# Kernel optimization log

Hardware: AMD Instinct MI355X
Metric: run time of the kernel (lower is better)

## Reference

```python
import jax, jax.numpy as jnp
import numpy as np

N, E, G = 50000, 800000, 64          # nodes, edges, graphs in batch
F, HG, HL = 64, 128, 128             # node feat, graph hidden, lin hidden
AVG_LOG = float(np.log(9.0))         # from deg histogram [0]*8+[1]: log(8+1)


def setup_inputs() -> dict:
    key = jax.random.key(0)
    ks = jax.random.split(key, 24)
    def w(k, shape):
        return 0.1 * jax.random.normal(k, shape, jnp.float32)
    return {
        "x": jax.random.normal(ks[0], (N, F), jnp.float32),
        "edge_index": jax.random.randint(ks[1], (2, E), 0, N),
        "edge_attr": jax.random.normal(ks[2], (E, 1), jnp.float32),
        "batch": jnp.sort(jax.random.randint(ks[3], (N,), 0, G)),
        # PNAConv params (towers=1, pre_layers=1, post_layers=1, edge_dim=1)
        "W_edge": w(ks[4], (1, F)),      "b_edge": w(ks[5], (F,)),
        "W_pre": w(ks[6], (3 * F, F)),   "b_pre": w(ks[7], (F,)),
        "W_post": w(ks[8], (13 * F, HG)), "b_post": w(ks[9], (HG,)),
        "W_lin": w(ks[10], (HG, HG)),    "b_lin": w(ks[11], (HG,)),
        # bn1 / fc2 / bn2
        "g1": jnp.ones((HG,)), "be1": jnp.zeros((HG,)),
        "W2": w(ks[12], (HG, HL)), "b2": w(ks[13], (HL,)),
        "g2": jnp.ones((HL,)), "be2": jnp.zeros((HL,)),
        # one resnet block: fc/bn/fc/bn
        "Wr1": w(ks[14], (HL, HL)), "br1": w(ks[15], (HL,)),
        "gr1": jnp.ones((HL,)), "ber1": jnp.zeros((HL,)),
        "Wr2": w(ks[16], (HL, HL)), "br2": w(ks[17], (HL,)),
        "gr2": jnp.ones((HL,)), "ber2": jnp.zeros((HL,)),
        "W_out": w(ks[18], (HL, 1)), "b_out": w(ks[19], (1,)),
    }


def _bn(z, g, b):
    # BatchNorm1d, training mode: biased batch stats, eps=1e-5
    mu = z.mean(0)
    var = ((z - mu) ** 2).mean(0)
    return (z - mu) * jax.lax.rsqrt(var + 1e-5) * g + b


def _pna(x, edge_index, edge_attr, W_edge, b_edge, W_pre, b_pre,
         W_post, b_post, W_lin, b_lin):
    src, dst = edge_index[0], edge_index[1]  # messages flow j->i, aggregate at dst
    e = edge_attr @ W_edge + b_edge                               # [E, F]
    m = jnp.concatenate([x[dst], x[src], e], -1) @ W_pre + b_pre  # [E, F]
    ones_e = jnp.ones((m.shape[0],), m.dtype)
    cnt = jax.ops.segment_sum(ones_e, dst, N)                     # in-degree
    cnt1 = jnp.maximum(cnt, 1.0)
    mean = jax.ops.segment_sum(m, dst, N) / cnt1[:, None]
    mean2 = jax.ops.segment_sum(m * m, dst, N) / cnt1[:, None]
    std = jnp.sqrt(jax.nn.relu(mean2 - mean * mean) + 1e-5)
    has = (cnt > 0)[:, None]
    mn = jnp.where(has, jax.ops.segment_min(m, dst, N), 0.0)
    mx = jnp.where(has, jax.ops.segment_max(m, dst, N), 0.0)
    agg = jnp.concatenate([mean, mn, mx, std], -1)                # [N, 4F]
    amp = (jnp.log(cnt1 + 1.0) / AVG_LOG)[:, None]                # amplification scaler
    out = jnp.concatenate([agg, agg * amp, agg / amp], -1)        # [N, 12F]
    out = jnp.concatenate([x, out], -1) @ W_post + b_post         # [N, HG]
    return out @ W_lin + b_lin                                    # [N, HG]


def reference(x, edge_index, edge_attr, batch,
              W_edge, b_edge, W_pre, b_pre, W_post, b_post, W_lin, b_lin,
              g1, be1, W2, b2, g2, be2,
              Wr1, br1, gr1, ber1, Wr2, br2, gr2, ber2,
              W_out, b_out):
    h = _pna(x, edge_index, edge_attr, W_edge, b_edge, W_pre, b_pre,
             W_post, b_post, W_lin, b_lin)
    # global_mean_pool over graphs
    gc = jnp.maximum(jax.ops.segment_sum(jnp.ones((h.shape[0],), h.dtype), batch, G), 1.0)
    z = jax.ops.segment_sum(h, batch, G) / gc[:, None]            # [G, HG]
    z = jax.nn.relu(_bn(z, g1, be1))
    z = jax.nn.relu(_bn(z @ W2 + b2, g2, be2))
    r = z
    z = jax.nn.relu(_bn(z @ Wr1 + br1, gr1, ber1))
    z = jax.nn.relu(_bn(z @ Wr2 + br2, gr2, ber2) + r)
    return z @ W_out + b_out                                      # [G, 1]
```

## Files before the change

kernel.cpp:

```cpp
#include <hip/hip_runtime.h>
#include <hip/hip_bf16.h>

using bf16 = __hip_bfloat16;

#define F 64
#define HG 128
#define HL 128
#define AVG_LOG_INV 0.45511961331341866f
#define BSH 5
#define BNODES 32
#define BCAP 1024
#define BTILE 8192
#define NBMAX 1664
#define NBTMAX 128

typedef short short8 __attribute__((ext_vector_type(8)));
typedef float floatx4 __attribute__((ext_vector_type(4)));

__device__ __forceinline__ float b2f(bf16 v) { return __bfloat162float(v); }
__device__ __forceinline__ bf16 f2b(float v) { return __float2bfloat16(v); }
__device__ __forceinline__ short f2bs(float v) { bf16 h = f2b(v); return *(short*)&h; }

__device__ __forceinline__ unsigned packbf2(float x, float y) {
    bf16 a = f2b(x), b = f2b(y);
    unsigned short ua = *(unsigned short*)&a, ub = *(unsigned short*)&b;
    return ((unsigned)ub << 16) | (unsigned)ua;
}

__device__ __forceinline__ float wave_sum(float v) {
    #pragma unroll
    for (int m = 32; m > 0; m >>= 1) v += __shfl_xor(v, m);
    return v;
}

__global__ __launch_bounds__(512) void k_prep(
    const float* __restrict__ x, const float* __restrict__ W_pre,
    bf16* __restrict__ AB, int N,
    const int* __restrict__ ei, const float* __restrict__ ea,
    int* __restrict__ ofs, int2* __restrict__ gout, int E,
    float* __restrict__ gfeat, int* __restrict__ gcnt,
    int NB, int GF, int G, int NBT,
    const float* __restrict__ W_edge, const float* __restrict__ b_edge,
    const float* __restrict__ b_pre, float* __restrict__ uc) {
    __shared__ __align__(16) char smem[18432];
    int t = threadIdx.x;
    int gtid = blockIdx.x * 512 + t;
    int gstr = gridDim.x * 512;
    for (int i = gtid; i < GF; i += gstr) gfeat[i] = 0.f;
    for (int i = gtid; i < G; i += gstr) gcnt[i] = 0;

    if (blockIdx.x < NBT) {
        int* hist = (int*)smem;
        int* aux  = hist + NBMAX;
        int p = blockIdx.x;
        for (int i = t; i < NB; i += 512) hist[i] = 0;
        __syncthreads();
        int base = p * BTILE;
        int lim = E - base; if (lim > BTILE) lim = BTILE;
        int nq = lim >> 2;
        const int4* dst4 = (const int4*)(ei + E + base);
        for (int q = t; q < nq; q += 512) {
            int4 d = dst4[q];
            atomicAdd(&hist[d.x >> BSH], 1);
            atomicAdd(&hist[d.y >> BSH], 1);
            atomicAdd(&hist[d.z >> BSH], 1);
            atomicAdd(&hist[d.w >> BSH], 1);
        }
        for (int i = (nq << 2) + t; i < lim; i += 512)
            atomicAdd(&hist[ei[E + base + i] >> BSH], 1);
        __syncthreads();
        int b0 = t * 4;
        int c0 = 0, c1 = 0, c2 = 0, c3 = 0;
        if (b0 < NB)     c0 = hist[b0];
        if (b0 + 1 < NB) c1 = hist[b0 + 1];
        if (b0 + 2 < NB) c2 = hist[b0 + 2];
        if (b0 + 3 < NB) c3 = hist[b0 + 3];
        int tot = c0 + c1 + c2 + c3;
        aux[t] = tot;
        __syncthreads();
        for (int d = 1; d < 512; d <<= 1) {
            int v = (t >= d) ? aux[t - d] : 0;
            __syncthreads();
            aux[t] += v;
            __syncthreads();
        }
        int run = aux[t] - tot;
        __syncthreads();
        size_t orow = (size_t)p * (NB + 1);
        if (b0 < NB)     { hist[b0]     = run; ofs[orow + b0]     = run; run += c0; }
        if (b0 + 1 < NB) { hist[b0 + 1] = run; ofs[orow + b0 + 1] = run; run += c1; }
        if (b0 + 2 < NB) { hist[b0 + 2] = run; ofs[orow + b0 + 2] = run; run += c2; }
        if (b0 + 3 < NB) { hist[b0 + 3] = run; ofs[orow + b0 + 3] = run; run += c3; }
        if (t == 0) ofs[orow + NB] = lim;
        for (int i = t; i < NB; i += 512) aux[i] = 0;
        __syncthreads();
        const int4* src4 = (const int4*)(ei + base);
        const float4* ea4 = (const float4*)(ea + base);
        int2* seg = gout + (size_t)p * BTILE;
        for (int q = t; q < nq; q += 512) {
            int4 s = src4[q], d = dst4[q];
            float4 v = ea4[q];
            int bb, pos;
            bb = d.x >> BSH; pos = hist[bb] + atomicAdd(&aux[bb], 1);
            seg[pos] = make_int2((d.x << 16) | s.x, __float_as_int(v.x));
            bb = d.y >> BSH; pos = hist[bb] + atomicAdd(&aux[bb], 1);
            seg[pos] = make_int2((d.y << 16) | s.y, __float_as_int(v.y));
            bb = d.z >> BSH; pos = hist[bb] + atomicAdd(&aux[bb], 1);
            seg[pos] = make_int2((d.z << 16) | s.z, __float_as_int(v.z));
            bb = d.w >> BSH; pos = hist[bb] + atomicAdd(&aux[bb], 1);
            seg[pos] = make_int2((d.w << 16) | s.w, __float_as_int(v.w));
        }
        for (int i = (nq << 2) + t; i < lim; i += 512) {
            int s = ei[base + i], d = ei[E + base + i];
            int bb = d >> BSH;
            int pos = hist[bb] + atomicAdd(&aux[bb], 1);
            seg[pos] = make_int2((d << 16) | s, __float_as_int(ea[base + i]));
        }
    } else {
        if (blockIdx.x == NBT && t < 64) {
            int f = t;
            float u = 0.f, c = b_pre[f];
            for (int k = 0; k < 64; k++) {
                float w3 = W_pre[(128 + k) * 64 + f];
                u += W_edge[k] * w3;
                c += b_edge[k] * w3;
            }
            uc[f] = u; uc[64 + f] = c;
        }
        unsigned short* wt = (unsigned short*)smem;
        for (int idx = t; idx < 8192; idx += 512) {
            int k = idx >> 7, m = idx & 127;
            float v = W_pre[((m & 64) + k) * 64 + (m & 63)];
            wt[m * 72 + k] = (unsigned short)f2bs(v);
        }
        __syncthreads();

        int lane = t & 63;
        int row = lane & 15, quad = lane >> 4;
        int w = (blockIdx.x - NBT) * 8 + (t >> 6);
        int nwaves = (gridDim.x - NBT) * 8;
        int ntiles = (N + 15) >> 4;

        for (int tile = w; tile < ntiles; tile += nwaves) {
            int m0 = tile << 4;
            int node_a = m0 + row; if (node_a >= N) node_a = N - 1;
            short8 a[2];
            #pragma unroll
            for (int h = 0; h < 2; h++) {
                const float* xp = x + (size_t)node_a * 64 + h * 32 + quad * 8;
                floatx4 v0 = *(const floatx4*)xp;
                floatx4 v1 = *(const floatx4*)(xp + 4);
                #pragma unroll
                for (int j = 0; j < 4; j++) { a[h][j] = f2bs(v0[j]); a[h][4 + j] = f2bs(v1[j]); }
            }
            #pragma unroll
            for (int tt = 0; tt < 8; tt++) {
                int fbase = tt * 16;
                floatx4 c = {0.f, 0.f, 0.f, 0.f};
                #pragma unroll
                for (int h = 0; h < 2; h++) {
                    short8 bfr = *(const short8*)(wt + (fbase + row) * 72 + h * 32 + quad * 8);
                    c = __builtin_amdgcn_mfma_f32_16x16x32_bf16(a[h], bfr, c, 0, 0, 0);
                }
                #pragma unroll
                for (int r = 0; r < 4; r++) {
                    int node = m0 + quad * 4 + r;
                    if (node < N) AB[(size_t)node * 128 + fbase + row] = f2b(c[r]);
                }
            }
        }
    }
}

__global__ __launch_bounds__(512) void k_edge(
    const bf16* __restrict__ AB, const int2* __restrict__ gout,
    const int* __restrict__ ofs, const float* __restrict__ uc,
    const int* __restrict__ batch, const float* __restrict__ x,
    float* __restrict__ gfeat, int* __restrict__ gcnt,
    int N, int NB, int NBT) {
    __shared__ int2 recs[BCAP], sortd[BCAP];
    __shared__ int ncnt[BNODES], nofs[BNODES], nrank[BNODES];
    __shared__ int gid[BNODES];
    __shared__ unsigned lstat[BNODES][128];
    __shared__ float lamp[BNODES], liamp[BNODES];
    __shared__ int runlo[NBTMAX], runlen[NBTMAX], runpre[NBTMAX];
    __shared__ int etot_s;
    int t = threadIdx.x;
    int b = blockIdx.x;
    int nn = N - b * BNODES; if (nn > BNODES) nn = BNODES;

    if (t < NBTMAX) { runlo[t] = 0; runlen[t] = 0; }
    if (t < BNODES) {
        ncnt[t] = 0; nrank[t] = 0;
        if (t < nn) gid[t] = batch[b * BNODES + t];
    }
    __syncthreads();
    if (t < NBT) {
        int lo = ofs[(size_t)t * (NB + 1) + b];
        int hi = ofs[(size_t)t * (NB + 1) + b + 1];
        runlo[t] = lo; runlen[t] = hi - lo;
    }
    __syncthreads();
    if (t < NBTMAX) runpre[t] = runlen[t];
    __syncthreads();
    for (int d = 1; d < NBTMAX; d <<= 1) {
        int v = 0;
        if (t < NBTMAX && t >= d) v = runpre[t - d];
        __syncthreads();
        if (t < NBTMAX) runpre[t] += v;
        __syncthreads();
    }
    if (t == NBTMAX - 1) etot_s = runpre[NBTMAX - 1];
    int ex = 0;
    if (t < NBTMAX) ex = runpre[t] - runlen[t];
    __syncthreads();
    if (t < NBTMAX) runpre[t] = ex;
    __syncthreads();
    int ecnt = etot_s; if (ecnt > BCAP) ecnt = BCAP;
    for (int i = t; i < ecnt; i += 512) {
        int lo2 = 0, hi2 = NBT;
        while (hi2 - lo2 > 1) {
            int mid = (lo2 + hi2) >> 1;
            if (runpre[mid] <= i) lo2 = mid; else hi2 = mid;
        }
        recs[i] = gout[(size_t)lo2 * BTILE + runlo[lo2] + (i - runpre[lo2])];
    }
    __syncthreads();
    for (int i = t; i < ecnt; i += 512)
        atomicAdd(&ncnt[((unsigned)recs[i].x >> 16) & (BNODES - 1)], 1);
    __syncthreads();
    if (t < BNODES) {
        int v = ncnt[t], inc = v;
        #pragma unroll
        for (int m = 1; m < BNODES; m <<= 1) { int u = __shfl_up(inc, m); if (t >= m) inc += u; }
        nofs[t] = inc - v;
    }
    __syncthreads();
    for (int i = t; i < ecnt; i += 512) {
        int2 r = recs[i];
        int nl = ((unsigned)r.x >> 16) & (BNODES - 1);
        int k = atomicAdd(&nrank[nl], 1);
        sortd[nofs[nl] + k] = r;
    }
    __syncthreads();

    int lane = t & 63, w = t >> 6;
    int half = lane & 31, hi32 = lane >> 5;
    float2 u2 = *(const float2*)(uc + 2 * half);
    float2 c2 = *(const float2*)(uc + 64 + 2 * half);

    for (int nl = w; nl < nn; nl += 8) {
        int n = b * BNODES + nl;
        int lo = nofs[nl], cnt = ncnt[nl], hi = lo + cnt;

        unsigned apack = *(const unsigned*)(AB + (size_t)n * 128 + 2 * half);
        float acx = __uint_as_float(apack << 16) + c2.x;
        float acy = __uint_as_float(apack & 0xffff0000u) + c2.y;

        float sx = 0.f, sy = 0.f, qx = 0.f, qy = 0.f;
        float mnx = 3.4e38f, mny = 3.4e38f, mxx = -3.4e38f, mxy = -3.4e38f;

        auto acc2 = [&](unsigned bp, float eav) {
            float bx = __uint_as_float(bp << 16);
            float by = __uint_as_float(bp & 0xffff0000u);
            float m0 = fmaf(eav, u2.x, acx) + bx;
            float m1 = fmaf(eav, u2.y, acy) + by;
            sx += m0; qx = fmaf(m0, m0, qx);
            sy += m1; qy = fmaf(m1, m1, qy);
            mnx = fminf(mnx, m0); mxx = fmaxf(mxx, m0);
            mny = fminf(mny, m1); mxy = fmaxf(mxy, m1);
        };
        auto gaddr = [&](int sn) {
            return (const unsigned*)(AB + (size_t)sn * 128 + 64 + 2 * half);
        };

        for (int base = lo; base < hi; base += 64) {
            int nb = hi - base; if (nb > 64) nb = 64;
            int2 rec = (lane < nb) ? sortd[base + lane] : make_int2(0, 0);
            int vsn = rec.x & 0xFFFF;
            float vea = __int_as_float(rec.y);
            int i = 0;
            for (; i + 8 <= nb; i += 8) {
                int sn0 = __shfl(vsn, i + hi32);
                int sn1 = __shfl(vsn, i + 2 + hi32);
                int sn2 = __shfl(vsn, i + 4 + hi32);
                int sn3 = __shfl(vsn, i + 6 + hi32);
                float e0 = __shfl(vea, i + hi32);
                float e1 = __shfl(vea, i + 2 + hi32);
                float e2 = __shfl(vea, i + 4 + hi32);
                float e3 = __shfl(vea, i + 6 + hi32);
                unsigned b0 = *gaddr(sn0);
                unsigned b1 = *gaddr(sn1);
                unsigned b2 = *gaddr(sn2);
                unsigned b3 = *gaddr(sn3);
                acc2(b0, e0); acc2(b1, e1); acc2(b2, e2); acc2(b3, e3);
            }
            for (; i + 2 <= nb; i += 2) {
                int   sn = __shfl(vsn, i + hi32);
                float ev = __shfl(vea, i + hi32);
                acc2(*gaddr(sn), ev);
            }
            if (i < nb) {
                int   sn = __shfl(vsn, i);
                float ev = __shfl(vea, i);
                unsigned bp = *gaddr(sn);
                if (hi32 == 0) acc2(bp, ev);
            }
        }
        sx += __shfl_xor(sx, 32); sy += __shfl_xor(sy, 32);
        qx += __shfl_xor(qx, 32); qy += __shfl_xor(qy, 32);
        mnx = fminf(mnx, __shfl_xor(mnx, 32)); mny = fminf(mny, __shfl_xor(mny, 32));
        mxx = fmaxf(mxx, __shfl_xor(mxx, 32)); mxy = fmaxf(mxy, __shfl_xor(mxy, 32));

        float c1 = (cnt > 0) ? (float)cnt : 1.f;
        float inv = 1.f / c1;
        float mex = sx * inv, mey = sy * inv;
        float vx = qx * inv - mex * mex; if (vx < 0.f) vx = 0.f;
        float vy = qy * inv - mey * mey; if (vy < 0.f) vy = 0.f;
        float sdx = sqrtf(vx + 1e-5f), sdy = sqrtf(vy + 1e-5f);
        if (cnt == 0) { mnx = mny = mxx = mxy = 0.f; }

        if (hi32 == 0) {
            lstat[nl][half]      = packbf2(mex, mey);
            lstat[nl][32 + half] = packbf2(mnx, mny);
        } else {
            lstat[nl][64 + half] = packbf2(mxx, mxy);
            lstat[nl][96 + half] = packbf2(sdx, sdy);
        }
        if (lane == 0) {
            float amp = logf(c1 + 1.f) * AVG_LOG_INV;
            lamp[nl] = amp; liamp[nl] = 1.f / amp;
        }
    }
    __syncthreads();

    if (t < 128) {
        int c = t;
        int elem = ((c >> 5) << 6) + ((c & 31) << 1);
        float s1x = 0.f, s1y = 0.f, s2x = 0.f, s2y = 0.f, s3x = 0.f, s3y = 0.f;
        float sxv = 0.f;
        int cnt = 0;
        int cur = gid[0];
        for (int nl = 0; nl < nn; nl++) {
            int g = gid[nl];
            if (g != cur) {
                float* gf = gfeat + (size_t)cur * 832;
                unsafeAtomicAdd(&gf[64 + elem], s1x);
                unsafeAtomicAdd(&gf[65 + elem], s1y);
                unsafeAtomicAdd(&gf[320 + elem], s2x);
                unsafeAtomicAdd(&gf[321 + elem], s2y);
                unsafeAtomicAdd(&gf[576 + elem], s3x);
                unsafeAtomicAdd(&gf[577 + elem], s3y);
                if (t < 64) unsafeAtomicAdd(&gf[t], sxv);
                if (t == 0) atomicAdd(&gcnt[cur], cnt);
                s1x = s1y = s2x = s2y = s3x = s3y = 0.f; sxv = 0.f; cnt = 0;
                cur = g;
            }
            unsigned p = lstat[nl][c];
            float bx = __uint_as_float(p << 16);
            float by = __uint_as_float(p & 0xffff0000u);
            float a = lamp[nl], ia = liamp[nl];
            s1x += bx; s2x = fmaf(bx, a, s2x); s3x = fmaf(bx, ia, s3x);
            s1y += by; s2y = fmaf(by, a, s2y); s3y = fmaf(by, ia, s3y);
            if (t < 64) sxv += x[(size_t)(b * BNODES + nl) * 64 + t];
            cnt++;
        }
        float* gf = gfeat + (size_t)cur * 832;
        unsafeAtomicAdd(&gf[64 + elem], s1x);
        unsafeAtomicAdd(&gf[65 + elem], s1y);
        unsafeAtomicAdd(&gf[320 + elem], s2x);
        unsafeAtomicAdd(&gf[321 + elem], s2y);
        unsafeAtomicAdd(&gf[576 + elem], s3x);
        unsafeAtomicAdd(&gf[577 + elem], s3y);
        if (t < 64) unsafeAtomicAdd(&gf[t], sxv);
        if (t == 0) atomicAdd(&gcnt[cur], cnt);
    }
}

__global__ void k_post1(const float* __restrict__ gfeat, const int* __restrict__ gcnt,
                        const float* __restrict__ W_post, const float* __restrict__ b_post,
                        const float* __restrict__ W_lin, const float* __restrict__ b_lin,
                        float* __restrict__ Zin) {
    int g = blockIdx.x, t = threadIdx.x;
    int j = t & 127, h = t >> 7;
    __shared__ float feat[832];
    __shared__ float part[256];
    __shared__ float z1[128];
    int cg = gcnt[g];
    float r = 1.f / ((cg > 0) ? (float)cg : 1.f);
    for (int i = t; i < 832; i += 256) feat[i] = gfeat[(size_t)g * 832 + i] * r;
    __syncthreads();
    float acc = (h == 0) ? b_post[j] : 0.f;
    const float* Wp = W_post + (size_t)(h * 416) * 128 + j;
    const float* fp = feat + h * 416;
    #pragma unroll 8
    for (int k = 0; k < 416; k++) acc += fp[k] * Wp[(size_t)k * 128];
    part[t] = acc;
    __syncthreads();
    if (t < 128) z1[j] = part[j] + part[128 + j];
    __syncthreads();
    float a2 = (h == 0) ? b_lin[j] : 0.f;
    #pragma unroll
    for (int k = 0; k < 64; k++) a2 += z1[h * 64 + k] * W_lin[(h * 64 + k) * 128 + j];
    part[t] = a2;
    __syncthreads();
    if (t < 128) {
        float v = part[j] + part[128 + j];
        if (cg == 0) v = 0.f;
        Zin[g * 128 + j] = v;
    }
}

__global__ void k_mlpcol(const float* __restrict__ in, const float* __restrict__ W,
                         const float* __restrict__ bias,
                         const float* __restrict__ gamma, const float* __restrict__ beta,
                         const float* __restrict__ res,
                         const float* __restrict__ g_in, const float* __restrict__ be_in,
                         float* __restrict__ outp) {
    __shared__ float A[64 * 129];
    __shared__ float part[4 * 64];
    int t = threadIdx.x;
    int j = blockIdx.x;

    for (int i = t; i < 8192; i += 256) A[(i >> 7) * 129 + (i & 127)] = in[i];
    __syncthreads();

    if (g_in) {
        if (t < 128) {
            int c = t;
            float mu = 0.f;
            for (int r = 0; r < 64; r++) mu += A[r * 129 + c];
            mu *= (1.f / 64.f);
            float var = 0.f;
            for (int r = 0; r < 64; r++) { float d = A[r * 129 + c] - mu; var += d * d; }
            var *= (1.f / 64.f);
            float sc = rsqrtf(var + 1e-5f) * g_in[c], sh = be_in[c];
            for (int r = 0; r < 64; r++) {
                float v = (A[r * 129 + c] - mu) * sc + sh;
                A[r * 129 + c] = v > 0.f ? v : 0.f;
            }
        }
        __syncthreads();
    }

    int r = t & 63, q = t >> 6;
    float acc = 0.f;
    int k0 = q * 32;
    #pragma unroll
    for (int k = 0; k < 32; k++) acc += A[r * 129 + k0 + k] * W[(k0 + k) * 128 + j];
    part[q * 64 + r] = acc;
    __syncthreads();

    if (t < 64) {
        float v = part[t] + part[64 + t] + part[128 + t] + part[192 + t] + bias[j];
        float mu = wave_sum(v) * (1.f / 64.f);
        float d = v - mu;
        float var = wave_sum(d * d) * (1.f / 64.f);
        float o = d * rsqrtf(var + 1e-5f) * gamma[j] + beta[j];
        if (res) o += res[t * 128 + j];
        outp[t * 128 + j] = o > 0.f ? o : 0.f;
    }
}

__global__ void k_out(const float* __restrict__ z4, const float* __restrict__ W_out,
                      const float* b_out, float* __restrict__ out) {
    int g = threadIdx.x;
    float acc = b_out[0];
    for (int j = 0; j < 128; j++) acc += z4[g * 128 + j] * W_out[j];
    out[g] = acc;
}

extern "C" void kernel_launch(void* const* d_in, const int* in_sizes, int n_in,
                              void* d_out, int out_size, void* d_ws, size_t ws_size,
                              hipStream_t stream) {
    const float* x      = (const float*)d_in[0];
    const int*   ei     = (const int*)d_in[1];
    const float* ea     = (const float*)d_in[2];
    const int*   batch  = (const int*)d_in[3];
    const float* W_edge = (const float*)d_in[4];
    const float* b_edge = (const float*)d_in[5];
    const float* W_pre  = (const float*)d_in[6];
    const float* b_pre  = (const float*)d_in[7];
    const float* W_post = (const float*)d_in[8];
    const float* b_post = (const float*)d_in[9];
    const float* W_lin  = (const float*)d_in[10];
    const float* b_lin  = (const float*)d_in[11];
    const float* g1     = (const float*)d_in[12];
    const float* be1    = (const float*)d_in[13];
    const float* W2     = (const float*)d_in[14];
    const float* b2     = (const float*)d_in[15];
    const float* g2     = (const float*)d_in[16];
    const float* be2    = (const float*)d_in[17];
    const float* Wr1    = (const float*)d_in[18];
    const float* br1    = (const float*)d_in[19];
    const float* gr1    = (const float*)d_in[20];
    const float* ber1   = (const float*)d_in[21];
    const float* Wr2    = (const float*)d_in[22];
    const float* br2    = (const float*)d_in[23];
    const float* gr2    = (const float*)d_in[24];
    const float* ber2   = (const float*)d_in[25];
    const float* W_out  = (const float*)d_in[26];
    const float* b_out  = (const float*)d_in[27];
    float* out = (float*)d_out;

    const int N = in_sizes[0] / F;
    const int E = in_sizes[1] / 2;
    const int G = out_size;
    const int NB = (N + BNODES - 1) >> BSH;

    char* p = (char*)d_ws;
    auto alloc = [&](size_t nbytes) { void* r = p; p += (nbytes + 255) & ~(size_t)255; return r; };
    const int NBT = (E + BTILE - 1) / BTILE;
    bf16*  AB     = (bf16*)alloc((size_t)N * 128 * sizeof(bf16));
    int2*  gout   = (int2*)alloc((size_t)NBT * BTILE * sizeof(int2));
    int*   ofs    = (int*)alloc((size_t)NBT * (NB + 1) * sizeof(int));
    float* uc     = (float*)alloc(128 * sizeof(float));
    float* gfeat  = (float*)alloc((size_t)G * 832 * sizeof(float));
    int*   gcnt   = (int*)alloc((size_t)G * sizeof(int));
    float* Zin    = (float*)alloc(64 * 128 * sizeof(float));
    float* z2b    = (float*)alloc(64 * 128 * sizeof(float));
    float* z3b    = (float*)alloc(64 * 128 * sizeof(float));
    float* z4b    = (float*)alloc(64 * 128 * sizeof(float));

    const int GF = G * 832;
    const int NAB = (((N + 15) >> 4) + 7) >> 3;

    k_prep<<<NBT + NAB, 512, 0, stream>>>(x, W_pre, AB, N, ei, ea, ofs, gout, E,
                                          gfeat, gcnt, NB, GF, G, NBT,
                                          W_edge, b_edge, b_pre, uc);
    k_edge<<<NB, 512, 0, stream>>>(AB, gout, ofs, uc, batch, x, gfeat, gcnt, N, NB, NBT);
    k_post1<<<G, 256, 0, stream>>>(gfeat, gcnt, W_post, b_post, W_lin, b_lin, Zin);
    k_mlpcol<<<HG, 256, 0, stream>>>(Zin, W2, b2, g2, be2, nullptr, g1, be1, z2b);
    k_mlpcol<<<HL, 256, 0, stream>>>(z2b, Wr1, br1, gr1, ber1, nullptr, nullptr, nullptr, z3b);
    k_mlpcol<<<HL, 256, 0, stream>>>(z3b, Wr2, br2, gr2, ber2, z2b, nullptr, nullptr, z4b);
    k_out<<<1, 64, 0, stream>>>(z4b, W_out, b_out, out);
}
```

Measured before the change: 227.0 us.

## Fuse MLP tail into one kernel, streamline edge-kernel setup and unroll gathers

The four tail kernels (three BN-MLP layers plus the output projection) become a single 1024-thread block kernel that keeps activations in shared memory and streams weight chunks. In k_edge, the shared-memory run prefix scan becomes a single-wave shuffle scan, record loading is fused with the per-node count atomics, and the gather loop gains a 16-wide unroll. The per-graph x-sum and node-count work moves from threads 0-63 and 0 onto otherwise idle threads. This cuts launch overhead, barriers and serialized work, at the cost of running the tail on one CU.

After: 271.9 us. 19.8% more time.

```diff
diff --git a/kernel.cpp b/kernel.cpp
--- a/kernel.cpp
+++ b/kernel.cpp
@@ -183,51 +183,49 @@
     __shared__ int gid[BNODES];
     __shared__ unsigned lstat[BNODES][128];
     __shared__ float lamp[BNODES], liamp[BNODES];
-    __shared__ int runlo[NBTMAX], runlen[NBTMAX], runpre[NBTMAX];
+    __shared__ int runlo[NBTMAX], runpre[NBTMAX];
     __shared__ int etot_s;
     int t = threadIdx.x;
     int b = blockIdx.x;
     int nn = N - b * BNODES; if (nn > BNODES) nn = BNODES;
 
-    if (t < NBTMAX) { runlo[t] = 0; runlen[t] = 0; }
-    if (t < BNODES) {
-        ncnt[t] = 0; nrank[t] = 0;
-        if (t < nn) gid[t] = batch[b * BNODES + t];
-    }
-    __syncthreads();
-    if (t < NBT) {
-        int lo = ofs[(size_t)t * (NB + 1) + b];
-        int hi = ofs[(size_t)t * (NB + 1) + b + 1];
-        runlo[t] = lo; runlen[t] = hi - lo;
-    }
-    __syncthreads();
-    if (t < NBTMAX) runpre[t] = runlen[t];
-    __syncthreads();
-    for (int d = 1; d < NBTMAX; d <<= 1) {
-        int v = 0;
-        if (t < NBTMAX && t >= d) v = runpre[t - d];
-        __syncthreads();
-        if (t < NBTMAX) runpre[t] += v;
-        __syncthreads();
-    }
-    if (t == NBTMAX - 1) etot_s = runpre[NBTMAX - 1];
-    int ex = 0;
-    if (t < NBTMAX) ex = runpre[t] - runlen[t];
-    __syncthreads();
-    if (t < NBTMAX) runpre[t] = ex;
-    __syncthreads();
+    if (t < 64) {
+        int l = t;
+        int p0 = 2 * l, p1 = 2 * l + 1;
+        int lo0 = 0, len0 = 0, lo1 = 0, len1 = 0;
+        if (p0 < NBT) {
+            lo0 = ofs[(size_t)p0 * (NB + 1) + b];
+            len0 = ofs[(size_t)p0 * (NB + 1) + b + 1] - lo0;
+        }
+        if (p1 < NBT) {
+            lo1 = ofs[(size_t)p1 * (NB + 1) + b];
+            len1 = ofs[(size_t)p1 * (NB + 1) + b + 1] - lo1;
+        }
+        runlo[p0] = lo0; runlo[p1] = lo1;
+        int s = len0 + len1, inc = s;
+        #pragma unroll
+        for (int m = 1; m < 64; m <<= 1) { int u = __shfl_up(inc, m); if (l >= m) inc += u; }
+        int ex = inc - s;
+        runpre[p0] = ex; runpre[p1] = ex + len0;
+        if (l == 63) etot_s = inc;
+    } else if (t < 96) {
+        int i = t - 64;
+        ncnt[i] = 0; nrank[i] = 0;
+        if (i < nn) gid[i] = batch[b * BNODES + i];
+    }
+    __syncthreads();
+
     int ecnt = etot_s; if (ecnt > BCAP) ecnt = BCAP;
     for (int i = t; i < ecnt; i += 512) {
-        int lo2 = 0, hi2 = NBT;
+        int lo2 = 0, hi2 = NBTMAX;
         while (hi2 - lo2 > 1) {
             int mid = (lo2 + hi2) >> 1;
             if (runpre[mid] <= i) lo2 = mid; else hi2 = mid;
         }
-        recs[i] = gout[(size_t)lo2 * BTILE + runlo[lo2] + (i - runpre[lo2])];
-    }
-    __syncthreads();
-    for (int i = t; i < ecnt; i += 512)
-        atomicAdd(&ncnt[((unsigned)recs[i].x >> 16) & (BNODES - 1)], 1);
+        int2 r = gout[(size_t)lo2 * BTILE + runlo[lo2] + (i - runpre[lo2])];
+        recs[i] = r;
+        atomicAdd(&ncnt[((unsigned)r.x >> 16) & (BNODES - 1)], 1);
+    }
     __syncthreads();
     if (t < BNODES) {
         int v = ncnt[t], inc = v;
@@ -280,6 +278,34 @@
             int vsn = rec.x & 0xFFFF;
             float vea = __int_as_float(rec.y);
             int i = 0;
+            for (; i + 16 <= nb; i += 16) {
+                int sn0 = __shfl(vsn, i + hi32);
+                int sn1 = __shfl(vsn, i + 2 + hi32);
+                int sn2 = __shfl(vsn, i + 4 + hi32);
+                int sn3 = __shfl(vsn, i + 6 + hi32);
+                int sn4 = __shfl(vsn, i + 8 + hi32);
+                int sn5 = __shfl(vsn, i + 10 + hi32);
+                int sn6 = __shfl(vsn, i + 12 + hi32);
+                int sn7 = __shfl(vsn, i + 14 + hi32);
+                float e0 = __shfl(vea, i + hi32);
+                float e1 = __shfl(vea, i + 2 + hi32);
+                float e2 = __shfl(vea, i + 4 + hi32);
+                float e3 = __shfl(vea, i + 6 + hi32);
+                float e4 = __shfl(vea, i + 8 + hi32);
+                float e5 = __shfl(vea, i + 10 + hi32);
+                float e6 = __shfl(vea, i + 12 + hi32);
+                float e7 = __shfl(vea, i + 14 + hi32);
+                unsigned b0 = *gaddr(sn0);
+                unsigned b1 = *gaddr(sn1);
+                unsigned b2 = *gaddr(sn2);
+                unsigned b3 = *gaddr(sn3);
+                unsigned b4 = *gaddr(sn4);
+                unsigned b5 = *gaddr(sn5);
+                unsigned b6 = *gaddr(sn6);
+                unsigned b7 = *gaddr(sn7);
+                acc2(b0, e0); acc2(b1, e1); acc2(b2, e2); acc2(b3, e3);
+                acc2(b4, e4); acc2(b5, e5); acc2(b6, e6); acc2(b7, e7);
+            }
             for (; i + 8 <= nb; i += 8) {
                 int sn0 = __shfl(vsn, i + hi32);
                 int sn1 = __shfl(vsn, i + 2 + hi32);
@@ -338,8 +364,6 @@
         int c = t;
         int elem = ((c >> 5) << 6) + ((c & 31) << 1);
         float s1x = 0.f, s1y = 0.f, s2x = 0.f, s2y = 0.f, s3x = 0.f, s3y = 0.f;
-        float sxv = 0.f;
-        int cnt = 0;
         int cur = gid[0];
         for (int nl = 0; nl < nn; nl++) {
             int g = gid[nl];
@@ -351,9 +375,7 @@
                 unsafeAtomicAdd(&gf[321 + elem], s2y);
                 unsafeAtomicAdd(&gf[576 + elem], s3x);
                 unsafeAtomicAdd(&gf[577 + elem], s3y);
-                if (t < 64) unsafeAtomicAdd(&gf[t], sxv);
-                if (t == 0) atomicAdd(&gcnt[cur], cnt);
-                s1x = s1y = s2x = s2y = s3x = s3y = 0.f; sxv = 0.f; cnt = 0;
+                s1x = s1y = s2x = s2y = s3x = s3y = 0.f;
                 cur = g;
             }
             unsigned p = lstat[nl][c];
@@ -362,8 +384,6 @@
             float a = lamp[nl], ia = liamp[nl];
             s1x += bx; s2x = fmaf(bx, a, s2x); s3x = fmaf(bx, ia, s3x);
             s1y += by; s2y = fmaf(by, a, s2y); s3y = fmaf(by, ia, s3y);
-            if (t < 64) sxv += x[(size_t)(b * BNODES + nl) * 64 + t];
-            cnt++;
         }
         float* gf = gfeat + (size_t)cur * 832;
         unsafeAtomicAdd(&gf[64 + elem], s1x);
@@ -372,8 +392,27 @@
         unsafeAtomicAdd(&gf[321 + elem], s2y);
         unsafeAtomicAdd(&gf[576 + elem], s3x);
         unsafeAtomicAdd(&gf[577 + elem], s3y);
-        if (t < 64) unsafeAtomicAdd(&gf[t], sxv);
-        if (t == 0) atomicAdd(&gcnt[cur], cnt);
+    } else if (t < 192) {
+        int c = t - 128;
+        float sxv = 0.f;
+        int cur = gid[0];
+        for (int nl = 0; nl < nn; nl++) {
+            int g = gid[nl];
+            if (g != cur) {
+                unsafeAtomicAdd(&gfeat[(size_t)cur * 832 + c], sxv);
+                sxv = 0.f; cur = g;
+            }
+            sxv += x[(size_t)(b * BNODES + nl) * 64 + c];
+        }
+        unsafeAtomicAdd(&gfeat[(size_t)cur * 832 + c], sxv);
+    } else if (t == 192) {
+        int cnt = 0, cur = gid[0];
+        for (int nl = 0; nl < nn; nl++) {
+            int g = gid[nl];
+            if (g != cur) { atomicAdd(&gcnt[cur], cnt); cnt = 0; cur = g; }
+            cnt++;
+        }
+        atomicAdd(&gcnt[cur], cnt);
     }
 }
 
@@ -411,63 +450,80 @@
     }
 }
 
-__global__ void k_mlpcol(const float* __restrict__ in, const float* __restrict__ W,
-                         const float* __restrict__ bias,
-                         const float* __restrict__ gamma, const float* __restrict__ beta,
-                         const float* __restrict__ res,
-                         const float* __restrict__ g_in, const float* __restrict__ be_in,
-                         float* __restrict__ outp) {
+__global__ __launch_bounds__(1024) void k_tail(
+    const float* __restrict__ Zin,
+    const float* __restrict__ g1, const float* __restrict__ be1,
+    const float* __restrict__ W2, const float* __restrict__ b2,
+    const float* __restrict__ g2, const float* __restrict__ be2,
+    const float* __restrict__ Wr1, const float* __restrict__ br1,
+    const float* __restrict__ gr1, const float* __restrict__ ber1,
+    const float* __restrict__ Wr2, const float* __restrict__ br2,
+    const float* __restrict__ gr2, const float* __restrict__ ber2,
+    const float* __restrict__ W_out, const float* __restrict__ b_out,
+    float* __restrict__ out) {
     __shared__ float A[64 * 129];
-    __shared__ float part[4 * 64];
+    __shared__ float Wc[32 * 128];
     int t = threadIdx.x;
-    int j = blockIdx.x;
-
-    for (int i = t; i < 8192; i += 256) A[(i >> 7) * 129 + (i & 127)] = in[i];
-    __syncthreads();
-
-    if (g_in) {
-        if (t < 128) {
-            int c = t;
-            float mu = 0.f;
-            for (int r = 0; r < 64; r++) mu += A[r * 129 + c];
-            mu *= (1.f / 64.f);
-            float var = 0.f;
-            for (int r = 0; r < 64; r++) { float d = A[r * 129 + c] - mu; var += d * d; }
-            var *= (1.f / 64.f);
-            float sc = rsqrtf(var + 1e-5f) * g_in[c], sh = be_in[c];
-            for (int r = 0; r < 64; r++) {
-                float v = (A[r * 129 + c] - mu) * sc + sh;
-                A[r * 129 + c] = v > 0.f ? v : 0.f;
-            }
-        }
-        __syncthreads();
-    }
-
-    int r = t & 63, q = t >> 6;
-    float acc = 0.f;
-    int k0 = q * 32;
+    int r = t & 63;
+    int w = t >> 6;
+    int j0 = w * 8;
+
+    float v[8], res[8];
     #pragma unroll
-    for (int k = 0; k < 32; k++) acc += A[r * 129 + k0 + k] * W[(k0 + k) * 128 + j];
-    part[q * 64 + r] = acc;
-    __syncthreads();
+    for (int jj = 0; jj < 8; jj++) v[jj] = Zin[r * 128 + j0 + jj];
+    #pragma unroll
+    for (int jj = 0; jj < 8; jj++) {
+        float mu = wave_sum(v[jj]) * (1.f / 64.f);
+        float d = v[jj] - mu;
+        float var = wave_sum(d * d) * (1.f / 64.f);
+        float o = d * rsqrtf(var + 1e-5f) * g1[j0 + jj] + be1[j0 + jj];
+        A[r * 129 + j0 + jj] = o > 0.f ? o : 0.f;
+    }
+    __syncthreads();
+
+    auto layer = [&](const float* W, const float* bias, const float* gamma,
+                     const float* beta, bool addres, bool saveres) {
+        float acc[8];
+        #pragma unroll
+        for (int jj = 0; jj < 8; jj++) acc[jj] = bias[j0 + jj];
+        for (int c = 0; c < 4; c++) {
+            for (int i = t; i < 4096; i += 1024) Wc[i] = W[c * 4096 + i];
+            __syncthreads();
+            #pragma unroll 8
+            for (int kk = 0; kk < 32; kk++) {
+                float av = A[r * 129 + c * 32 + kk];
+                #pragma unroll
+                for (int jj = 0; jj < 8; jj++) acc[jj] += av * Wc[kk * 128 + j0 + jj];
+            }
+            __syncthreads();
+        }
+        #pragma unroll
+        for (int jj = 0; jj < 8; jj++) {
+            float mu = wave_sum(acc[jj]) * (1.f / 64.f);
+            float d = acc[jj] - mu;
+            float var = wave_sum(d * d) * (1.f / 64.f);
+            float o = d * rsqrtf(var + 1e-5f) * gamma[j0 + jj] + beta[j0 + jj];
+            if (addres) o += res[jj];
+            o = o > 0.f ? o : 0.f;
+            if (saveres) res[jj] = o;
+            v[jj] = o;
+        }
+        __syncthreads();
+        #pragma unroll
+        for (int jj = 0; jj < 8; jj++) A[r * 129 + j0 + jj] = v[jj];
+        __syncthreads();
+    };
+
+    layer(W2, b2, g2, be2, false, true);
+    layer(Wr1, br1, gr1, ber1, false, false);
+    layer(Wr2, br2, gr2, ber2, true, false);
 
     if (t < 64) {
-        float v = part[t] + part[64 + t] + part[128 + t] + part[192 + t] + bias[j];
-        float mu = wave_sum(v) * (1.f / 64.f);
-        float d = v - mu;
-        float var = wave_sum(d * d) * (1.f / 64.f);
-        float o = d * rsqrtf(var + 1e-5f) * gamma[j] + beta[j];
-        if (res) o += res[t * 128 + j];
-        outp[t * 128 + j] = o > 0.f ? o : 0.f;
-    }
-}
-
-__global__ void k_out(const float* __restrict__ z4, const float* __restrict__ W_out,
-                      const float* b_out, float* __restrict__ out) {
-    int g = threadIdx.x;
-    float acc = b_out[0];
-    for (int j = 0; j < 128; j++) acc += z4[g * 128 + j] * W_out[j];
-    out[g] = acc;
+        float acc = b_out[0];
+        #pragma unroll 8
+        for (int j = 0; j < 128; j++) acc += A[t * 129 + j] * W_out[j];
+        out[t] = acc;
+    }
 }
 
 extern "C" void kernel_launch(void* const* d_in, const int* in_sizes, int n_in,
@@ -518,9 +574,6 @@
     float* gfeat  = (float*)alloc((size_t)G * 832 * sizeof(float));
     int*   gcnt   = (int*)alloc((size_t)G * sizeof(int));
     float* Zin    = (float*)alloc(64 * 128 * sizeof(float));
-    float* z2b    = (float*)alloc(64 * 128 * sizeof(float));
-    float* z3b    = (float*)alloc(64 * 128 * sizeof(float));
-    float* z4b    = (float*)alloc(64 * 128 * sizeof(float));
 
     const int GF = G * 832;
     const int NAB = (((N + 15) >> 4) + 7) >> 3;
@@ -530,8 +583,7 @@
                                           W_edge, b_edge, b_pre, uc);
     k_edge<<<NB, 512, 0, stream>>>(AB, gout, ofs, uc, batch, x, gfeat, gcnt, N, NB, NBT);
     k_post1<<<G, 256, 0, stream>>>(gfeat, gcnt, W_post, b_post, W_lin, b_lin, Zin);
-    k_mlpcol<<<HG, 256, 0, stream>>>(Zin, W2, b2, g2, be2, nullptr, g1, be1, z2b);
-    k_mlpcol<<<HL, 256, 0, stream>>>(z2b, Wr1, br1, gr1, ber1, nullptr, nullptr, nullptr, z3b);
-    k_mlpcol<<<HL, 256, 0, stream>>>(z3b, Wr2, br2, gr2, ber2, z2b, nullptr, nullptr, z4b);
-    k_out<<<1, 64, 0, stream>>>(z4b, W_out, b_out, out);
-}
+    k_tail<<<1, 1024, 0, stream>>>(Zin, g1, be1, W2, b2, g2, be2,
+                                   Wr1, br1, gr1, ber1, Wr2, br2, gr2, ber2,
+                                   W_out, b_out, out);
+}
```
